# Performance work log

Hardware: AMD Instinct MI355X
Metric: run time of the kernel (lower is better)

## Reference

```python
import jax, jax.numpy as jnp
import numpy as np

T, B, C = 4096, 8, 1024
H, K = 16, 31


def setup_inputs() -> dict:
    key = jax.random.key(0)
    k1, k2 = jax.random.split(key)
    x = jax.random.normal(k1, (T, B, C), dtype=jnp.float32)
    # kaiming-uniform-ish init on (H, 1, K)
    bound = float(np.sqrt(6.0 / K))
    weight = jax.random.uniform(k2, (H, 1, K), dtype=jnp.float32, minval=-bound, maxval=bound)
    return {"x": x, "weight": weight}


def reference(x, weight):
    # x: (T, B, C); weight: (H, 1, K) shared across R = C // H channels per head.
    T_, B_, C_ = x.shape
    H_, _, K_ = weight.shape
    R = C_ // H_
    pad_l = K_ // 2  # calc_padding for odd K
    # Expand head weights to per-channel depthwise filters: (C, 1, K)
    w = jnp.repeat(weight, R, axis=0)
    xb = jnp.transpose(x, (1, 2, 0))  # (B, C, T)
    # out[t] = sum_k w[k] * x[t - pad_l + k]  (cross-correlation, matching unfold1d)
    out = jax.lax.conv_general_dilated(
        xb, w,
        window_strides=(1,),
        padding=[(pad_l, K_ - 1 - pad_l)],
        feature_group_count=C_,
        dimension_numbers=("NCH", "OIH", "NCH"),
    )  # (B, C, T)
    return jnp.transpose(out, (2, 0, 1))  # (T, B, C)
```

## Files before the change

### kernel.cpp

```cpp
#include <hip/hip_runtime.h>


#define T_DIM 4096
#define B_DIM 8
#define C_DIM 1024
#define H_DIM 16
#define K_DIM 31
#define PAD   15
#define COLS  (B_DIM * C_DIM / 4)
#define CH    16
#define WIN   (K_DIM - 1 + CH)

__global__ __launch_bounds__(256)
void lconv_kernel(const float* __restrict__ x,
                  const float* __restrict__ w,
                  float* __restrict__ out) {
    __shared__ float lw[H_DIM * K_DIM];
    const int tid = threadIdx.x;
    for (int i = tid; i < H_DIM * K_DIM; i += 256) lw[i] = w[i];
    __syncthreads();

    const int col = blockIdx.x * 256 + tid;
    const int h   = (col & 255) >> 4;
    const int t0  = blockIdx.y * CH;

    const float4* xp = (const float4*)x + (long long)(t0 - PAD) * COLS + col;

    float4 win[WIN];

    if (t0 >= PAD && t0 + CH + PAD <= T_DIM) {
        #pragma unroll
        for (int i = 0; i < WIN; ++i)
            win[i] = xp[(long long)i * COLS];
    } else {
        #pragma unroll
        for (int i = 0; i < WIN; ++i) {
            const int t = t0 - PAD + i;
            win[i] = (t >= 0 && t < T_DIM) ? xp[(long long)i * COLS]
                                           : float4{0.f, 0.f, 0.f, 0.f};
        }
    }

    __builtin_amdgcn_sched_barrier(0);

    float wk[K_DIM];
    #pragma unroll
    for (int k = 0; k < K_DIM; ++k) wk[k] = lw[h * K_DIM + k];

    float4* op = (float4*)out + (long long)t0 * COLS + col;
    #pragma unroll
    for (int j = 0; j < CH; ++j) {
        float4 a = {0.f, 0.f, 0.f, 0.f};
        #pragma unroll
        for (int k = 0; k < K_DIM; ++k) {
            a.x = fmaf(wk[k], win[j + k].x, a.x);
            a.y = fmaf(wk[k], win[j + k].y, a.y);
            a.z = fmaf(wk[k], win[j + k].z, a.z);
            a.w = fmaf(wk[k], win[j + k].w, a.w);
        }
        op[(long long)j * COLS] = a;
    }
}

extern "C" void kernel_launch(void* const* d_in, const int* in_sizes, int n_in,
                              void* d_out, int out_size, void* d_ws, size_t ws_size,
                              hipStream_t stream) {
    const float* x = (const float*)d_in[0];
    const float* w = (const float*)d_in[1];
    float* out = (float*)d_out;

    dim3 grid(COLS / 256, T_DIM / CH);
    lconv_kernel<<<grid, 256, 0, stream>>>(x, w, out);
}
```

Measured before the change: 231.2 us.

## Double temporal chunk per thread and split window loads into two phases

Raises the per-thread time chunk from 16 to 32 outputs so each loaded input row is reused by more outputs, cutting the halo re-read overhead. Loads the first 46 rows, computes the first 16 outputs, then loads the remaining rows and computes the rest, so loads can overlap compute. The sched_barrier is removed and launch bounds now request 2 blocks per CU. The 61-float4 window plus 31 weights needs a very large register budget, which risks lower occupancy or spills.

```diff
diff --git a/kernel.cpp b/kernel.cpp
--- a/kernel.cpp
+++ b/kernel.cpp
@@ -8,10 +8,10 @@
 #define K_DIM 31
 #define PAD   15
 #define COLS  (B_DIM * C_DIM / 4)
-#define CH    16
+#define CH    32
 #define WIN   (K_DIM - 1 + CH)
 
-__global__ __launch_bounds__(256)
+__global__ __launch_bounds__(256, 2)
 void lconv_kernel(const float* __restrict__ x,
                   const float* __restrict__ w,
                   float* __restrict__ out) {
@@ -25,31 +25,57 @@
     const int t0  = blockIdx.y * CH;
 
     const float4* xp = (const float4*)x + (long long)(t0 - PAD) * COLS + col;
+    float4* op = (float4*)out + (long long)t0 * COLS + col;
+
+    const bool interior = (t0 >= PAD) && (t0 + CH + PAD <= T_DIM);
 
     float4 win[WIN];
 
-    if (t0 >= PAD && t0 + CH + PAD <= T_DIM) {
+    float wk[K_DIM];
+    #pragma unroll
+    for (int k = 0; k < K_DIM; ++k) wk[k] = lw[h * K_DIM + k];
+
+    if (interior) {
         #pragma unroll
-        for (int i = 0; i < WIN; ++i)
+        for (int i = 0; i < 46; ++i)
             win[i] = xp[(long long)i * COLS];
     } else {
         #pragma unroll
-        for (int i = 0; i < WIN; ++i) {
+        for (int i = 0; i < 46; ++i) {
             const int t = t0 - PAD + i;
             win[i] = (t >= 0 && t < T_DIM) ? xp[(long long)i * COLS]
                                            : float4{0.f, 0.f, 0.f, 0.f};
         }
     }
 
-    __builtin_amdgcn_sched_barrier(0);
+    #pragma unroll
+    for (int j = 0; j < 16; ++j) {
+        float4 a = {0.f, 0.f, 0.f, 0.f};
+        #pragma unroll
+        for (int k = 0; k < K_DIM; ++k) {
+            a.x = fmaf(wk[k], win[j + k].x, a.x);
+            a.y = fmaf(wk[k], win[j + k].y, a.y);
+            a.z = fmaf(wk[k], win[j + k].z, a.z);
+            a.w = fmaf(wk[k], win[j + k].w, a.w);
+        }
+        op[(long long)j * COLS] = a;
+    }
 
-    float wk[K_DIM];
+    if (interior) {
+        #pragma unroll
+        for (int i = 46; i < WIN; ++i)
+            win[i] = xp[(long long)i * COLS];
+    } else {
+        #pragma unroll
+        for (int i = 46; i < WIN; ++i) {
+            const int t = t0 - PAD + i;
+            win[i] = (t >= 0 && t < T_DIM) ? xp[(long long)i * COLS]
+                                           : float4{0.f, 0.f, 0.f, 0.f};
+        }
+    }
+
     #pragma unroll
-    for (int k = 0; k < K_DIM; ++k) wk[k] = lw[h * K_DIM + k];
-
-    float4* op = (float4*)out + (long long)t0 * COLS + col;
-    #pragma unroll
-    for (int j = 0; j < CH; ++j) {
+    for (int j = 16; j < CH; ++j) {
         float4 a = {0.f, 0.f, 0.f, 0.f};
         #pragma unroll
         for (int k = 0; k < K_DIM; ++k) {
```

After: 244.5 us. 1.06x slower.
